# Performance work log

Hardware: AMD Instinct MI355X
Metric: run time of the kernel (lower is better)

Reference implementation:

```python
import jax, jax.numpy as jnp
import numpy as np

STRIDE = (1, 2, 2)
PADDING = ((2, 2), (3, 3), (3, 3))


def setup_inputs() -> dict:
    key = jax.random.key(0)
    kx, kw, kb = jax.random.split(key, 3)
    x = jax.random.normal(kx, (8, 3, 16, 112, 112), dtype=jnp.float32)
    weight = jax.random.normal(kw, (64, 3, 5, 7, 7), dtype=jnp.float32)
    bias = jax.random.normal(kb, (64,), dtype=jnp.float32)
    return {"x": x, "weight": weight, "bias": bias}


def reference(x, weight, bias):
    # NCDHW input, OIDHW weight -> NCDHW output; same math as the
    # torch module's explicit slice-multiply-sum conv3d.
    out = jax.lax.conv_general_dilated(
        x, weight,
        window_strides=STRIDE,
        padding=PADDING,
        dimension_numbers=("NCDHW", "OIDHW", "NCDHW"),
    )
    out = out + bias[None, :, None, None, None]
    return out
```

## Files before the change

kernel.cpp:

```cpp
#include <hip/hip_runtime.h>


typedef __attribute__((ext_vector_type(8)))  short short8;
typedef __attribute__((ext_vector_type(4)))  float f32x4;
typedef __attribute__((ext_vector_type(16))) float f32x16;

#define CI 3
#define DI 16
#define HI 112
#define WI 112
#define CO 64
#define DO_ 16
#define HO 56
#define WO 56
#define HW_IN 12544
#define DHWO 50176

#define NROW 105
#define NCH 27

#define XP_ROW 144
#define XP_H   119
#define XP_D   20
#define XPAD_BYTES  (8*3*XP_D*XP_H*XP_ROW*2)
#define WBUF_OFF    XPAD_BYTES
#define WS_NEED     (WBUF_OFF + NCH*4*64*16 + 4096)

#define SEG_SH 1296
#define SEG_DW 648

__device__ __forceinline__ unsigned short f2bf(float f) {
    unsigned u = __float_as_uint(f);
    return (unsigned short)((u + 0x7FFFu + ((u >> 16) & 1u)) >> 16);
}
__device__ __forceinline__ unsigned pk_bf16(float a, float b) {
    unsigned r;
    asm("v_cvt_pk_bf16_f32 %0, %1, %2" : "=v"(r) : "v"(a), "v"(b));
    return r;
}

__device__ __forceinline__ constexpr int rb2(int r) {
    const int rc = (r > 104) ? 104 : r;
    const int c  = rc / 35;
    const int kd = (rc / 7) % 5;
    const int kh = rc % 7;
    return (c * 6 + kd) * SEG_DW + kh * (XP_ROW / 2);
}

#define XP_THREADS (8*3*XP_D*XP_H*18)
#define XP_BLOCKS  4017

__global__ void prep_all(const float* __restrict__ x, const float* __restrict__ wgt,
                         unsigned* __restrict__ xp, short8* __restrict__ wbuf) {
    if (blockIdx.x < XP_BLOCKS) {
        const int g = blockIdx.x * 256 + threadIdx.x;
        if (g >= XP_THREADS) return;
        const int s8 = g % 18;
        int r = g / 18;
        const int hp = r % XP_H; r /= XP_H;
        const int dp = r % XP_D; r /= XP_D;
        const int c  = r % 3;
        const int n  = r / 3;
        const int din = dp - 2, hin = hp - 3;
        const bool rowok = ((unsigned)din < (unsigned)DI) && ((unsigned)hin < (unsigned)HI);
        float v[8];
        const int w0 = 8 * s8 - 3;
        if (rowok && s8 >= 1 && s8 <= 13) {
            const float* xr = x + ((n * CI + c) * DI + din) * HW_IN + hin * WI + w0;
            #pragma unroll
            for (int j = 0; j < 8; ++j) v[j] = xr[j];
        } else if (rowok && (s8 == 0 || s8 == 14)) {
            const float* xr = x + ((n * CI + c) * DI + din) * HW_IN + hin * WI;
            #pragma unroll
            for (int j = 0; j < 8; ++j) {
                const int w = w0 + j;
                v[j] = ((unsigned)w < (unsigned)WI) ? xr[w] : 0.0f;
            }
        } else {
            #pragma unroll
            for (int j = 0; j < 8; ++j) v[j] = 0.0f;
        }
        uint4 o;
        o.x = pk_bf16(v[0], v[1]); o.y = pk_bf16(v[2], v[3]);
        o.z = pk_bf16(v[4], v[5]); o.w = pk_bf16(v[6], v[7]);
        *reinterpret_cast<uint4*>(xp + 4 * (size_t)g) = o;
    } else {
        const int t = (blockIdx.x - XP_BLOCKS) * 256 + threadIdx.x;
        const int lane = t & 63;
        const int cf   = t >> 6;
        const int q    = cf & 3;
        const int a    = q & 1;
        const int ks   = q >> 1;
        const int ch   = cf >> 2;
        const int l31  = lane & 31;
        const int hl   = lane >> 5;
        const int co   = a * 32 + l31;
        const int r    = ch * 4 + ks * 2 + hl;
        const int rc   = (r > 104) ? 104 : r;
        const int c    = rc / 35;
        const int kd   = (rc / 7) % 5;
        const int kh   = rc % 7;
        const float* wsrc = wgt + (((co * CI + c) * 5 + kd) * 7 + kh) * 7;
        short8 v;
        #pragma unroll
        for (int j = 0; j < 8; ++j) {
            float w = (r < NROW && j < 7) ? wsrc[j] : 0.0f;
            v[j] = (short)f2bf(w);
        }
        wbuf[(size_t)cf * 64 + lane] = v;
    }
}

#define MFMA32(A, B, C) __builtin_amdgcn_mfma_f32_32x32x16_bf16(A, B, C, 0, 0, 0)

__launch_bounds__(256, 3)
__global__ void conv3d_v10(const unsigned short* __restrict__ xpad,
                           const short8* __restrict__ wbuf,
                           const float* __restrict__ bias,
                           float* __restrict__ out) {
    __shared__ __align__(16) unsigned short xl[18 * SEG_SH];

    const int tid = threadIdx.x;
    int b = ((blockIdx.x & 7) * 224) + (blockIdx.x >> 3);
    const int ht  = b % 28;  b /= 28;
    const int ddp = b & 7;
    const int n   = b >> 3;
    const int ho0 = ht * 2;
    const int dd0 = ddp * 2;

    const int lane = tid & 63;
    const int wid  = tid >> 6;

    {
        const size_t nb = (size_t)(n * CI) * XP_D;
        for (int s = wid; s < 18; s += 4) {
            const int c = s / 6;
            const int p = s - c * 6;
            const char* gsrc = (const char*)(xpad +
                ((nb + (size_t)c * XP_D + (dd0 + p)) * XP_H + 2 * ho0) * XP_ROW)
                + lane * 16;
            char* ldst = (char*)&xl[s * SEG_SH];
            __builtin_amdgcn_global_load_lds(
                (const __attribute__((address_space(1))) void*)(gsrc),
                (__attribute__((address_space(3))) void*)(ldst), 16, 0, 0);
            __builtin_amdgcn_global_load_lds(
                (const __attribute__((address_space(1))) void*)(gsrc + 1024),
                (__attribute__((address_space(3))) void*)(ldst + 1024), 16, 0, 0);
            if (lane < 34)
                __builtin_amdgcn_global_load_lds(
                    (const __attribute__((address_space(1))) void*)(gsrc + 2048),
                    (__attribute__((address_space(3))) void*)(ldst + 2048), 16, 0, 0);
        }
    }
    __syncthreads();

    const int ddl = wid & 1;
    const int hoL = wid >> 1;
    const int l31 = lane & 31;
    const int hl  = lane >> 5;
    const int tspB = ddl * SEG_DW + hoL * 144 + l31;

    f32x16 acc[2][2];
    #pragma unroll
    for (int a = 0; a < 2; ++a) {
        f32x16 bv;
        #pragma unroll
        for (int g = 0; g < 16; ++g)
            bv[g] = bias[a * 32 + (g & 3) + 8 * (g >> 2) + 4 * hl];
        acc[a][0] = bv; acc[a][1] = bv;
    }

    const short8* wbp = wbuf + lane;
    const unsigned* xlu = reinterpret_cast<const unsigned*>(xl);

    union BxU { unsigned u[4]; short8 s; };
    short8 As[2][4];
    BxU    Bs[2][4];

    auto loadA = [&](int ch, int slot) {
        #pragma unroll
        for (int q = 0; q < 4; ++q) As[slot][q] = wbp[(ch * 4 + q) * 64];
    };
    auto loadB = [&](int ch, int slot) {
        #pragma unroll
        for (int ks = 0; ks < 2; ++ks) {
            const int r0 = ch * 4 + ks * 2;
            const int b0 = rb2(r0);
            const int b1 = rb2(r0 + 1);
            const int base = b0 + hl * (b1 - b0);
            const unsigned* xp = xlu + base + tspB;
            #pragma unroll
            for (int f = 0; f < 2; ++f) {
                const unsigned* p = xp + f * 32;
                Bs[slot][ks * 2 + f].u[0] = p[0];
                Bs[slot][ks * 2 + f].u[1] = p[1];
                Bs[slot][ks * 2 + f].u[2] = p[2];
                Bs[slot][ks * 2 + f].u[3] = p[3];
            }
        }
    };

    loadA(0, 0);
    loadB(0, 0);

    #pragma unroll
    for (int ch = 0; ch < NCH; ++ch) {
        if (ch + 1 < NCH) {
            loadA(ch + 1, (ch + 1) & 1);
            loadB(ch + 1, (ch + 1) & 1);
        }
        __builtin_amdgcn_sched_barrier(0);
        const int s = ch & 1;
        #pragma unroll
        for (int a = 0; a < 2; ++a) {
            #pragma unroll
            for (int f = 0; f < 2; ++f) {
                acc[a][f] = MFMA32(As[s][0 + a], Bs[s][0 + f].s, acc[a][f]);
                acc[a][f] = MFMA32(As[s][2 + a], Bs[s][2 + f].s, acc[a][f]);
            }
        }
        __builtin_amdgcn_sched_barrier(0);
    }

    const int dd = dd0 + ddl;
    const int ho = ho0 + hoL;
    const size_t obase = (size_t)n * CO * DHWO + (size_t)dd * 3136 + ho * WO;
    #pragma unroll
    for (int f = 0; f < 2; ++f) {
        const int wo = f * 32 + l31;
        if (f == 0 || l31 < 24) {
            #pragma unroll
            for (int a = 0; a < 2; ++a) {
                #pragma unroll
                for (int g = 0; g < 16; ++g) {
                    const int co = a * 32 + (g & 3) + 8 * (g >> 2) + 4 * hl;
                    out[obase + (size_t)co * DHWO + wo] = acc[a][f][g];
                }
            }
        }
    }
}

#define FB_LR 13
#define FB_LROWS 234
#define FB_LWS 144
#define FB_XLSZ (FB_LROWS*FB_LWS)
#define MFMA16(A, B, C) __builtin_amdgcn_mfma_f32_16x16x32_bf16(A, B, C, 0, 0, 0)

__global__ void prep_weights_fb(const float* __restrict__ wgt, short8* __restrict__ wbuf) {
    const int t    = blockIdx.x * 64 + threadIdx.x;
    const int lane = t & 63;
    const int cf   = t >> 6;
    const int l15  = lane & 15;
    const int kgrp = lane >> 4;
    const int co   = (cf & 3) * 16 + l15;
    const int rr   = (cf >> 2) * 4 + kgrp;
    const int rc   = (rr < NROW) ? rr : (NROW - 1);
    const int c    = rc / 35;
    const int kd   = (rc / 7) % 5;
    const int kh   = rc % 7;
    const float* wsrc = wgt + (((co * CI + c) * 5 + kd) * 7 + kh) * 7;
    short8 v;
    #pragma unroll
    for (int j = 0; j < 8; ++j) {
        float w = (rr < NROW && j < 7) ? wsrc[j] : 0.0f;
        v[j] = (short)f2bf(w);
    }
    wbuf[(size_t)cf * 64 + lane] = v;
}

__launch_bounds__(512, 2)
__global__ void conv3d_mfma4(const float* __restrict__ x,
                             const short8* __restrict__ wbuf,
                             const float* __restrict__ bias,
                             float* __restrict__ out) {
    __shared__ unsigned short xl[FB_XLSZ];
    __shared__ int rowg[FB_LROWS];
    __shared__ unsigned short tabr[108];

    const int tid = threadIdx.x;
    int b = blockIdx.x;
    const int ht  = b % 14;  b /= 14;
    const int ddp = b % 8;
    const int n   = b / 8;
    const int ho0 = ht * 4;
    const int dd0 = ddp * 2;

    if (tid < FB_LROWS) {
        const int c   = tid / (6 * FB_LR);
        const int rem = tid - c * (6 * FB_LR);
        const int p   = rem / FB_LR;
        const int rl  = rem - p * FB_LR;
        const int din = dd0 - 2 + p;
        const int hin = 2 * ho0 - 3 + rl;
        const bool ok = ((unsigned)din < (unsigned)DI) && ((unsigned)hin < (unsigned)HI);
        rowg[tid] = ok ? ((n * CI + c) * DI + din) * HW_IN + hin * WI : -1;
    }
    if (tid < 108) {
        const int rc = (tid < NROW) ? tid : (NROW - 1);
        const int c  = rc / 35;
        const int kd = (rc / 7) % 5;
        const int kh = rc % 7;
        tabr[tid] = (unsigned short)(((c * 6 + kd) * FB_LR + kh) * FB_LWS);
    }
    __syncthreads();

    const int lane = tid & 63;
    const int wid  = tid >> 6;

    for (int row = wid; row < FB_LROWS; row += 8) {
        const int base = rowg[row];
        unsigned short* dst = &xl[row * FB_LWS];
        if (lane < 57) {
            float v0 = 0.0f, v1 = 0.0f;
            const int w0 = 2 * lane - 1;
            if (base >= 0) {
                if (lane >= 1)  v0 = x[base + w0];
                if (lane <= 55) v1 = x[base + w0 + 1];
            }
            *reinterpret_cast<unsigned*>(&dst[2 * lane + 2]) = pk_bf16(v0, v1);
        } else {
            const int dw = (lane == 57) ? 0 : lane;
            *reinterpret_cast<unsigned*>(&dst[2 * dw]) = 0u;
        }
    }
    __syncthreads();

    const int ddl  = wid & 1;
    const int hoL  = wid >> 1;
    const int l15  = lane & 15;
    const int kgrp = lane >> 4;
    const int woff = ddl * (FB_LR * FB_LWS) + hoL * (2 * FB_LWS);

    f32x4 acc[4][4];
    #pragma unroll
    for (int a = 0; a < 4; ++a) {
        f32x4 bv;
        #pragma unroll
        for (int r = 0; r < 4; ++r) bv[r] = bias[a * 16 + kgrp * 4 + r];
        #pragma unroll
        for (int f = 0; f < 4; ++f) acc[a][f] = bv;
    }

    const short8* wbp = wbuf + lane;
    short8 Acur[4], Anxt[4];
    #pragma unroll
    for (int a = 0; a < 4; ++a) Acur[a] = wbp[a * 64];
    int tb = (int)tabr[kgrp] + woff;

    const unsigned* xlu = reinterpret_cast<const unsigned*>(xl);

    for (int ch = 0; ch < NCH; ++ch) {
        int tbn = 0;
        if (ch + 1 < NCH) {
            tbn = (int)tabr[(ch + 1) * 4 + kgrp] + woff;
            #pragma unroll
            for (int a = 0; a < 4; ++a) Anxt[a] = wbp[((ch + 1) * 4 + a) * 64];
        }
        const unsigned* xp = xlu + (tb >> 1) + l15;
        union { unsigned u[4]; short8 s; } bx[4];
        #pragma unroll
        for (int f = 0; f < 4; ++f) {
            const unsigned* p = xp + f * 16;
            bx[f].u[0] = p[0]; bx[f].u[1] = p[1];
            bx[f].u[2] = p[2]; bx[f].u[3] = p[3];
        }
        #pragma unroll
        for (int f = 0; f < 4; ++f) {
            acc[0][f] = MFMA16(Acur[0], bx[f].s, acc[0][f]);
            acc[1][f] = MFMA16(Acur[1], bx[f].s, acc[1][f]);
            acc[2][f] = MFMA16(Acur[2], bx[f].s, acc[2][f]);
            acc[3][f] = MFMA16(Acur[3], bx[f].s, acc[3][f]);
        }
        tb = tbn;
        #pragma unroll
        for (int a = 0; a < 4; ++a) Acur[a] = Anxt[a];
    }

    const int dd = dd0 + ddl;
    const int ho = ho0 + hoL;
    #pragma unroll
    for (int f = 0; f < 4; ++f) {
        const int wo = f * 16 + l15;
        if (f < 3 || l15 < 8) {
            float* op = out + (((size_t)(n * CO) * DO_ + dd) * HO + ho) * WO + wo;
            #pragma unroll
            for (int a = 0; a < 4; ++a) {
                const int co = a * 16 + kgrp * 4;
                #pragma unroll
                for (int r = 0; r < 4; ++r)
                    op[(size_t)(co + r) * DHWO] = acc[a][f][r];
            }
        }
    }
}

extern "C" void kernel_launch(void* const* d_in, const int* in_sizes, int n_in,
                              void* d_out, int out_size, void* d_ws, size_t ws_size,
                              hipStream_t stream) {
    const float* x    = (const float*)d_in[0];
    const float* wgt  = (const float*)d_in[1];
    const float* bias = (const float*)d_in[2];
    float* out        = (float*)d_out;

    if (ws_size >= (size_t)WS_NEED) {
        unsigned* xpad = (unsigned*)d_ws;
        short8* wbuf   = (short8*)((char*)d_ws + WBUF_OFF);
        hipLaunchKernelGGL(prep_all, dim3(XP_BLOCKS + 27, 1, 1), dim3(256, 1, 1), 0,
                           stream, x, wgt, xpad, wbuf);
        hipLaunchKernelGGL(conv3d_v10, dim3(1792, 1, 1), dim3(256, 1, 1), 0, stream,
                           (const unsigned short*)xpad, wbuf, bias, out);
    } else {
        short8* wbuf = (short8*)d_ws;
        hipLaunchKernelGGL(prep_weights_fb, dim3(NCH * 4, 1, 1), dim3(64, 1, 1), 0,
                           stream, wgt, wbuf);
        hipLaunchKernelGGL(conv3d_mfma4, dim3(896, 1, 1), dim3(512, 1, 1), 0, stream,
                           x, wbuf, bias, out);
    }
}
```

Before: 67.44 us.

## Split conv block work across 8 waves, one wo-half per wave

Doubles the block to 512 threads so each wave computes one 32-wide half of the output row instead of both, which halves the per-wave accumulators and B-fragment registers to allow higher occupancy. The last chunk skips the zero-padded half K-step, the barrier moves after the first weight prefetch, and MFMA sections run at raised wave priority. Each block now has twice as many waves issuing duplicate weight (A) loads, and the second half of each row wastes 8 of 32 lanes on padding.

Measured after the change: 78.47 us. +16.4%, slower.

```diff
diff --git a/kernel.cpp b/kernel.cpp
--- a/kernel.cpp
+++ b/kernel.cpp
@@ -113,8 +113,8 @@
 
 #define MFMA32(A, B, C) __builtin_amdgcn_mfma_f32_32x32x16_bf16(A, B, C, 0, 0, 0)
 
-__launch_bounds__(256, 3)
-__global__ void conv3d_v10(const unsigned short* __restrict__ xpad,
+__launch_bounds__(512, 4)
+__global__ void conv3d_v12(const unsigned short* __restrict__ xpad,
                            const short8* __restrict__ wbuf,
                            const float* __restrict__ bias,
                            float* __restrict__ out) {
@@ -133,7 +133,7 @@
 
     {
         const size_t nb = (size_t)(n * CI) * XP_D;
-        for (int s = wid; s < 18; s += 4) {
+        for (int s = wid; s < 18; s += 8) {
             const int c = s / 6;
             const int p = s - c * 6;
             const char* gsrc = (const char*)(xpad +
@@ -152,22 +152,22 @@
                     (__attribute__((address_space(3))) void*)(ldst + 2048), 16, 0, 0);
         }
     }
-    __syncthreads();
 
     const int ddl = wid & 1;
-    const int hoL = wid >> 1;
+    const int hoL = (wid >> 1) & 1;
+    const int woH = wid >> 2;
     const int l31 = lane & 31;
     const int hl  = lane >> 5;
-    const int tspB = ddl * SEG_DW + hoL * 144 + l31;
-
-    f32x16 acc[2][2];
+    const int tspB = ddl * SEG_DW + hoL * 144 + woH * 32 + l31;
+
+    f32x16 acc[2];
     #pragma unroll
     for (int a = 0; a < 2; ++a) {
         f32x16 bv;
         #pragma unroll
         for (int g = 0; g < 16; ++g)
             bv[g] = bias[a * 32 + (g & 3) + 8 * (g >> 2) + 4 * hl];
-        acc[a][0] = bv; acc[a][1] = bv;
+        acc[a] = bv;
     }
 
     const short8* wbp = wbuf + lane;
@@ -175,32 +175,34 @@
 
     union BxU { unsigned u[4]; short8 s; };
     short8 As[2][4];
-    BxU    Bs[2][4];
+    BxU    Bs[2][2];
 
     auto loadA = [&](int ch, int slot) {
-        #pragma unroll
-        for (int q = 0; q < 4; ++q) As[slot][q] = wbp[(ch * 4 + q) * 64];
+        const int nq = (ch == NCH - 1) ? 2 : 4;
+        #pragma unroll
+        for (int q = 0; q < 4; ++q)
+            if (q < nq) As[slot][q] = wbp[(ch * 4 + q) * 64];
     };
     auto loadB = [&](int ch, int slot) {
+        const int nks = (ch == NCH - 1) ? 1 : 2;
         #pragma unroll
         for (int ks = 0; ks < 2; ++ks) {
-            const int r0 = ch * 4 + ks * 2;
-            const int b0 = rb2(r0);
-            const int b1 = rb2(r0 + 1);
-            const int base = b0 + hl * (b1 - b0);
-            const unsigned* xp = xlu + base + tspB;
-            #pragma unroll
-            for (int f = 0; f < 2; ++f) {
-                const unsigned* p = xp + f * 32;
-                Bs[slot][ks * 2 + f].u[0] = p[0];
-                Bs[slot][ks * 2 + f].u[1] = p[1];
-                Bs[slot][ks * 2 + f].u[2] = p[2];
-                Bs[slot][ks * 2 + f].u[3] = p[3];
+            if (ks < nks) {
+                const int r0 = ch * 4 + ks * 2;
+                const int b0 = rb2(r0);
+                const int b1 = rb2(r0 + 1);
+                const int base = b0 + hl * (b1 - b0);
+                const unsigned* xp = xlu + base + tspB;
+                Bs[slot][ks].u[0] = xp[0];
+                Bs[slot][ks].u[1] = xp[1];
+                Bs[slot][ks].u[2] = xp[2];
+                Bs[slot][ks].u[3] = xp[3];
             }
         }
     };
 
     loadA(0, 0);
+    __syncthreads();
     loadB(0, 0);
 
     #pragma unroll
@@ -210,32 +212,29 @@
             loadB(ch + 1, (ch + 1) & 1);
         }
         __builtin_amdgcn_sched_barrier(0);
+        __builtin_amdgcn_s_setprio(1);
         const int s = ch & 1;
         #pragma unroll
         for (int a = 0; a < 2; ++a) {
-            #pragma unroll
-            for (int f = 0; f < 2; ++f) {
-                acc[a][f] = MFMA32(As[s][0 + a], Bs[s][0 + f].s, acc[a][f]);
-                acc[a][f] = MFMA32(As[s][2 + a], Bs[s][2 + f].s, acc[a][f]);
-            }
-        }
+            acc[a] = MFMA32(As[s][0 + a], Bs[s][0].s, acc[a]);
+            if (ch != NCH - 1)
+                acc[a] = MFMA32(As[s][2 + a], Bs[s][1].s, acc[a]);
+        }
+        __builtin_amdgcn_s_setprio(0);
         __builtin_amdgcn_sched_barrier(0);
     }
 
     const int dd = dd0 + ddl;
     const int ho = ho0 + hoL;
+    const int wo = woH * 32 + l31;
     const size_t obase = (size_t)n * CO * DHWO + (size_t)dd * 3136 + ho * WO;
-    #pragma unroll
-    for (int f = 0; f < 2; ++f) {
-        const int wo = f * 32 + l31;
-        if (f == 0 || l31 < 24) {
-            #pragma unroll
-            for (int a = 0; a < 2; ++a) {
-                #pragma unroll
-                for (int g = 0; g < 16; ++g) {
-                    const int co = a * 32 + (g & 3) + 8 * (g >> 2) + 4 * hl;
-                    out[obase + (size_t)co * DHWO + wo] = acc[a][f][g];
-                }
+    if (wo < WO) {
+        #pragma unroll
+        for (int a = 0; a < 2; ++a) {
+            #pragma unroll
+            for (int g = 0; g < 16; ++g) {
+                const int co = a * 32 + (g & 3) + 8 * (g >> 2) + 4 * hl;
+                out[obase + (size_t)co * DHWO + wo] = acc[a][g];
             }
         }
     }
@@ -408,7 +407,7 @@
         short8* wbuf   = (short8*)((char*)d_ws + WBUF_OFF);
         hipLaunchKernelGGL(prep_all, dim3(XP_BLOCKS + 27, 1, 1), dim3(256, 1, 1), 0,
                            stream, x, wgt, xpad, wbuf);
-        hipLaunchKernelGGL(conv3d_v10, dim3(1792, 1, 1), dim3(256, 1, 1), 0, stream,
+        hipLaunchKernelGGL(conv3d_v12, dim3(1792, 1, 1), dim3(512, 1, 1), 0, stream,
                            (const unsigned short*)xpad, wbuf, bias, out);
     } else {
         short8* wbuf = (short8*)d_ws;
```
